# Kernel tuning notes

Hardware: AMD Instinct MI355X
Metric: run time of the kernel (lower is better)

Reference implementation:

```python
import jax, jax.numpy as jnp
import numpy as np


def setup_inputs() -> dict:
    key = jax.random.key(0)
    k1, k2 = jax.random.split(key)
    N, D, n_bags, per_bag = 8192, 512, 64, 128
    features = jax.random.normal(k1, (N, D), dtype=jnp.float32)
    # sorted bag indicator: 64 bags x 128 instances each
    batch = jnp.repeat(jnp.arange(n_bags, dtype=jnp.int32), per_bag)
    W = jax.random.normal(k2, (D, D), dtype=jnp.float32) * np.float32(1.0 / np.sqrt(D))
    b = jnp.zeros((D,), dtype=jnp.float32)
    return {"features": features, "W": W, "b": b, "batch": batch, "n_topk": 16, "n_bags": n_bags}


def reference(features, W, b, batch, n_topk, n_bags):
    N = features.shape[0]
    # F.normalize(dim=1): x / max(||x||, eps)
    norm = jnp.sqrt(jnp.sum(features * features, axis=1, keepdims=True))
    nf = features / jnp.maximum(norm, 1e-12)
    corr = nf @ nf.T  # [N, N] cosine-similarity map
    same_bag = batch[:, None] == batch[None, :]
    adj = jnp.where(same_bag, corr, 0.0)
    # scatter-zero the (N - n_topk) smallest per row == keep n_topk largest per row
    _, top_idx = jax.lax.top_k(adj, n_topk)  # [N, n_topk]
    keep = jnp.zeros((N, N), dtype=bool).at[jnp.arange(N)[:, None], top_idx].set(True)
    adj = jnp.where(keep, adj, 0.0)
    # dense_to_sparse()[0] keeps only indices -> unit edge weights for GCNConv.
    # GCNConv (gcn_norm, add_self_loops=True): A_hat = binarized adjacency with diag forced to 1.
    eye = jnp.eye(N, dtype=bool)
    A = jnp.where(eye, 1.0, (adj != 0).astype(features.dtype))  # [N, N]
    deg = jnp.sum(A, axis=0)  # degree scattered on target (col) index in PyG
    dis = jax.lax.rsqrt(deg)  # deg >= 1 thanks to self loops
    xw = features @ W  # [N, D]
    # out[col] = d[col]^-1/2 * sum_row A[row,col] * d[row]^-1/2 * xw[row]
    gcn_out = dis[:, None] * (A.T @ (dis[:, None] * xw)) + b
    # one-hot^T @ features == per-bag segment sum
    agg = jax.ops.segment_sum(gcn_out, batch, num_segments=n_bags)  # [n_bags, D]
    return agg, adj
```

## Files before the change

### kernel.cpp

```cpp
#include <hip/hip_runtime.h>
#include <hip/hip_bf16.h>

#define N 8192
#define D 512
#define NBAGS 64
#define PER_BAG 128
#define TOPK 16

typedef float vfloat4 __attribute__((ext_vector_type(4)));

#define WS_INVN   0
#define WS_KIDX   32768
#define WS_KCNT   557056
#define WS_DEG    589824

__global__ void norm_kernel(const float* __restrict__ feat,
                            float* __restrict__ invn,
                            int* __restrict__ deg) {
    int t = threadIdx.x;
    if (blockIdx.x < 32) deg[blockIdx.x * 256 + t] = 0;
    int lane = t & 63, w = t >> 6;
    int r = blockIdx.x * 4 + w;
    const float4* fr = (const float4*)(feat + (size_t)r * D);
    float4 a = fr[lane];
    float4 bq = fr[lane + 64];
    float ss = a.x * a.x + a.y * a.y + a.z * a.z + a.w * a.w
             + bq.x * bq.x + bq.y * bq.y + bq.z * bq.z + bq.w * bq.w;
    #pragma unroll
    for (int off = 32; off > 0; off >>= 1) ss += __shfl_down(ss, off);
    if (lane == 0) invn[r] = 1.0f / fmaxf(sqrtf(ss), 1e-12f);
}

__global__ __launch_bounds__(256, 1) void simtopk_kernel(
        const float* __restrict__ feat,
        const float* __restrict__ invn,
        float* __restrict__ adjOut,
        int* __restrict__ keptIdx,
        int* __restrict__ keptCnt,
        int* __restrict__ deg) {
    int rg = blockIdx.x;
    int bag = blockIdx.y;
    int t = threadIdx.x;
    __shared__ float colT[32][132];
    __shared__ float rowT[32][36];
    int bagBase = bag * PER_BAG;
    int rowBase = bagBase + rg * 32;
    int tx = t & 31;
    int ty = t >> 5;
    float4 acc[4];
    #pragma unroll
    for (int i = 0; i < 4; ++i) acc[i] = make_float4(0.f, 0.f, 0.f, 0.f);

    int kk = t & 31;
    int sub = t >> 5;
    int zrh = t >> 7;
    int zc  = t & 127;
    int jw  = bag >> 2;
    int winLo = bag * 32, winHi = winLo + 32;
    vfloat4 zf4 = {0.f, 0.f, 0.f, 0.f};

    for (int it = 0; it < 16; ++it) {
        int k0 = it * 32;
        __syncthreads();
        #pragma unroll
        for (int c0 = 0; c0 < 16; ++c0) {
            int c = sub * 16 + c0;
            colT[kk][c] = feat[(size_t)(bagBase + c) * D + k0 + kk];
        }
        #pragma unroll
        for (int r0 = 0; r0 < 4; ++r0) {
            int r = sub * 4 + r0;
            rowT[kk][r] = feat[(size_t)(rowBase + r) * D + k0 + kk];
        }
        __syncthreads();
        {
            int zr = 2 * it + zrh;
            vfloat4* rowp = (vfloat4*)(adjOut + (size_t)(rowBase + zr) * N);
            #pragma unroll
            for (int j = 0; j < 16; ++j) {
                int f = zc + 128 * j;
                if (j == jw) {
                    if (f < winLo || f >= winHi)
                        __builtin_nontemporal_store(zf4, &rowp[f]);
                } else {
                    __builtin_nontemporal_store(zf4, &rowp[f]);
                }
            }
        }
        #pragma unroll
        for (int k = 0; k < 32; ++k) {
            float4 cv = *(const float4*)&colT[k][4 * tx];
            float4 rv = *(const float4*)&rowT[k][4 * ty];
            acc[0].x += rv.x * cv.x; acc[0].y += rv.x * cv.y;
            acc[0].z += rv.x * cv.z; acc[0].w += rv.x * cv.w;
            acc[1].x += rv.y * cv.x; acc[1].y += rv.y * cv.y;
            acc[1].z += rv.y * cv.z; acc[1].w += rv.y * cv.w;
            acc[2].x += rv.z * cv.x; acc[2].y += rv.z * cv.y;
            acc[2].z += rv.z * cv.z; acc[2].w += rv.z * cv.w;
            acc[3].x += rv.w * cv.x; acc[3].y += rv.w * cv.y;
            acc[3].z += rv.w * cv.z; acc[3].w += rv.w * cv.w;
        }
    }
    float ic0 = invn[bagBase + 4 * tx];
    float ic1 = invn[bagBase + 4 * tx + 1];
    float ic2 = invn[bagBase + 4 * tx + 2];
    float ic3 = invn[bagBase + 4 * tx + 3];
    #pragma unroll
    for (int i = 0; i < 4; ++i) {
        float ir = invn[rowBase + 4 * ty + i];
        acc[i].x *= ir * ic0; acc[i].y *= ir * ic1;
        acc[i].z *= ir * ic2; acc[i].w *= ir * ic3;
    }
    #pragma unroll
    for (int i = 0; i < 4; ++i) {
        int r = rowBase + 4 * ty + i;
        float o0 = acc[i].x, o1 = acc[i].y, o2 = acc[i].z, o3 = acc[i].w;
        float w0 = o0, w1 = o1, w2 = o2, w3 = o3;
        int pm = 0, cnt = 0;
        #pragma unroll 1
        for (int itk = 0; itk < TOPK; ++itk) {
            float bv = w0; int bj = 0;
            if (w1 > bv) { bv = w1; bj = 1; }
            if (w2 > bv) { bv = w2; bj = 2; }
            if (w3 > bv) { bv = w3; bj = 3; }
            int bi = 4 * tx + bj;
            #pragma unroll
            for (int s = 1; s < 32; s <<= 1) {
                float ov = __shfl_xor(bv, s);
                int oi = __shfl_xor(bi, s);
                if (ov > bv || (ov == bv && oi < bi)) { bv = ov; bi = oi; }
            }
            if (bv <= 0.0f) break;
            if (tx == 0) keptIdx[(size_t)r * TOPK + cnt] = bi;
            cnt++;
            if ((bi >> 2) == tx) {
                pm |= 1 << (bi & 3);
                int q = bi & 3;
                if (q == 0) w0 = -1e30f;
                else if (q == 1) w1 = -1e30f;
                else if (q == 2) w2 = -1e30f;
                else w3 = -1e30f;
            }
        }
        if (tx == 0) keptCnt[r] = cnt;
        float4 ov4 = make_float4((pm & 1) ? o0 : 0.0f,
                                 (pm & 2) ? o1 : 0.0f,
                                 (pm & 4) ? o2 : 0.0f,
                                 (pm & 8) ? o3 : 0.0f);
        *(float4*)(adjOut + (size_t)r * N + bagBase + 4 * tx) = ov4;
        if (pm & 1) atomicAdd(&deg[bagBase + 4 * tx], 1);
        if (pm & 2) atomicAdd(&deg[bagBase + 4 * tx + 1], 1);
        if (pm & 4) atomicAdd(&deg[bagBase + 4 * tx + 2], 1);
        if (pm & 8) atomicAdd(&deg[bagBase + 4 * tx + 3], 1);
        int selfCol = rg * 32 + 4 * ty + i;
        if (tx == (selfCol >> 2) && !((pm >> (selfCol & 3)) & 1))
            atomicAdd(&deg[bagBase + selfCol], 1);
    }
}

__global__ void wfwagg_kernel(const float* __restrict__ feat,
                              const int* __restrict__ keptIdx,
                              const int* __restrict__ keptCnt,
                              const int* __restrict__ deg,
                              const float* __restrict__ Wm,
                              const float* __restrict__ b,
                              float* __restrict__ aggOut) {
    int bag = blockIdx.x;
    int t = threadIdx.x;
    __shared__ float wsh[PER_BAG];
    __shared__ float fws[D];
    int bagBase = bag * PER_BAG;
    if (t < PER_BAG) {
        int r = bagBase + t;
        int cnt = keptCnt[r];
        float sum = 0.0f;
        bool selfin = false;
        for (int k = 0; k < cnt; ++k) {
            int c = keptIdx[(size_t)r * TOPK + k];
            if (c == t) selfin = true;
            sum += rsqrtf((float)deg[bagBase + c]);
        }
        float disr = rsqrtf((float)deg[r]);
        if (!selfin) sum += disr;
        wsh[t] = disr * sum;
    }
    __syncthreads();
    float acc = 0.0f;
    #pragma unroll 8
    for (int r = 0; r < PER_BAG; ++r)
        acc += wsh[r] * feat[(size_t)(bagBase + r) * D + t];
    fws[t] = acc;
    __syncthreads();
    float acc2 = 0.0f;
    #pragma unroll 8
    for (int k = 0; k < D; ++k)
        acc2 += fws[k] * Wm[(size_t)k * D + t];
    aggOut[bag * D + t] = acc2 + 128.0f * b[t];
}

extern "C" void kernel_launch(void* const* d_in, const int* in_sizes, int n_in,
                              void* d_out, int out_size, void* d_ws, size_t ws_size,
                              hipStream_t stream) {
    const float* feat = (const float*)d_in[0];
    const float* Wm   = (const float*)d_in[1];
    const float* b    = (const float*)d_in[2];

    char* ws = (char*)d_ws;
    float* invn   = (float*)(ws + WS_INVN);
    int* keptIdx  = (int*)(ws + WS_KIDX);
    int* keptCnt  = (int*)(ws + WS_KCNT);
    int* deg      = (int*)(ws + WS_DEG);

    float* aggOut = (float*)d_out;
    float* adjOut = (float*)d_out + NBAGS * D;

    norm_kernel<<<N / 4, 256, 0, stream>>>(feat, invn, deg);
    simtopk_kernel<<<dim3(4, NBAGS), 256, 0, stream>>>(feat, invn, adjOut,
                                                       keptIdx, keptCnt, deg);
    wfwagg_kernel<<<NBAGS, 512, 0, stream>>>(feat, keptIdx, keptCnt, deg,
                                             Wm, b, aggOut);
}
```

Baseline: 367.5 us.

## Double-buffer similarity tile loads and split aggregation into parallel kernels

The similarity/top-k kernel now prefetches the next k-slice into registers with vectorized float4 loads while computing on a double-buffered shared tile, which removes one barrier per iteration and overlaps global loads with FMAs. The final weighted-feature and W projection stage is split into two kernels with more blocks (64x4 and 64x2) so more CUs participate instead of only 64 blocks. The split adds an extra kernel launch and a workspace round-trip for the intermediate vector.

New measurement: 371.4 us. No clear change (+1.1%).

```diff
diff --git a/kernel.cpp b/kernel.cpp
--- a/kernel.cpp
+++ b/kernel.cpp
@@ -13,6 +13,7 @@
 #define WS_KIDX   32768
 #define WS_KCNT   557056
 #define WS_DEG    589824
+#define WS_FW     622592
 
 __global__ void norm_kernel(const float* __restrict__ feat,
                             float* __restrict__ invn,
@@ -41,38 +42,60 @@
     int rg = blockIdx.x;
     int bag = blockIdx.y;
     int t = threadIdx.x;
-    __shared__ float colT[32][132];
-    __shared__ float rowT[32][36];
+    __shared__ float colT[2][32][132];
+    __shared__ float rowT[2][32][36];
     int bagBase = bag * PER_BAG;
     int rowBase = bagBase + rg * 32;
     int tx = t & 31;
     int ty = t >> 5;
+    const float4* feat4 = (const float4*)feat;
+
+    int cC[4], cKq[4];
+    #pragma unroll
+    for (int i = 0; i < 4; ++i) {
+        int fidx = i * 256 + t;
+        cC[i] = fidx >> 3;
+        cKq[i] = fidx & 7;
+    }
+    int rR = t >> 3, rKq = t & 7;
+
     float4 acc[4];
     #pragma unroll
     for (int i = 0; i < 4; ++i) acc[i] = make_float4(0.f, 0.f, 0.f, 0.f);
 
-    int kk = t & 31;
-    int sub = t >> 5;
     int zrh = t >> 7;
     int zc  = t & 127;
     int jw  = bag >> 2;
     int winLo = bag * 32, winHi = winLo + 32;
     vfloat4 zf4 = {0.f, 0.f, 0.f, 0.f};
 
+    float4 pc[4], pr;
+    #pragma unroll
+    for (int i = 0; i < 4; ++i)
+        pc[i] = feat4[(size_t)(bagBase + cC[i]) * 128 + cKq[i]];
+    pr = feat4[(size_t)(rowBase + rR) * 128 + rKq];
+
+    int buf = 0;
     for (int it = 0; it < 16; ++it) {
-        int k0 = it * 32;
+        #pragma unroll
+        for (int i = 0; i < 4; ++i) {
+            colT[buf][cKq[i] * 4 + 0][cC[i]] = pc[i].x;
+            colT[buf][cKq[i] * 4 + 1][cC[i]] = pc[i].y;
+            colT[buf][cKq[i] * 4 + 2][cC[i]] = pc[i].z;
+            colT[buf][cKq[i] * 4 + 3][cC[i]] = pc[i].w;
+        }
+        rowT[buf][rKq * 4 + 0][rR] = pr.x;
+        rowT[buf][rKq * 4 + 1][rR] = pr.y;
+        rowT[buf][rKq * 4 + 2][rR] = pr.z;
+        rowT[buf][rKq * 4 + 3][rR] = pr.w;
         __syncthreads();
-        #pragma unroll
-        for (int c0 = 0; c0 < 16; ++c0) {
-            int c = sub * 16 + c0;
-            colT[kk][c] = feat[(size_t)(bagBase + c) * D + k0 + kk];
-        }
-        #pragma unroll
-        for (int r0 = 0; r0 < 4; ++r0) {
-            int r = sub * 4 + r0;
-            rowT[kk][r] = feat[(size_t)(rowBase + r) * D + k0 + kk];
-        }
-        __syncthreads();
+        if (it < 15) {
+            int kq0 = (it + 1) * 8;
+            #pragma unroll
+            for (int i = 0; i < 4; ++i)
+                pc[i] = feat4[(size_t)(bagBase + cC[i]) * 128 + kq0 + cKq[i]];
+            pr = feat4[(size_t)(rowBase + rR) * 128 + kq0 + rKq];
+        }
         {
             int zr = 2 * it + zrh;
             vfloat4* rowp = (vfloat4*)(adjOut + (size_t)(rowBase + zr) * N);
@@ -87,19 +110,24 @@
                 }
             }
         }
-        #pragma unroll
-        for (int k = 0; k < 32; ++k) {
-            float4 cv = *(const float4*)&colT[k][4 * tx];
-            float4 rv = *(const float4*)&rowT[k][4 * ty];
-            acc[0].x += rv.x * cv.x; acc[0].y += rv.x * cv.y;
-            acc[0].z += rv.x * cv.z; acc[0].w += rv.x * cv.w;
-            acc[1].x += rv.y * cv.x; acc[1].y += rv.y * cv.y;
-            acc[1].z += rv.y * cv.z; acc[1].w += rv.y * cv.w;
-            acc[2].x += rv.z * cv.x; acc[2].y += rv.z * cv.y;
-            acc[2].z += rv.z * cv.z; acc[2].w += rv.z * cv.w;
-            acc[3].x += rv.w * cv.x; acc[3].y += rv.w * cv.y;
-            acc[3].z += rv.w * cv.z; acc[3].w += rv.w * cv.w;
-        }
+        {
+            const float (*cT)[132] = colT[buf];
+            const float (*rT)[36]  = rowT[buf];
+            #pragma unroll
+            for (int k = 0; k < 32; ++k) {
+                float4 cv = *(const float4*)&cT[k][4 * tx];
+                float4 rv = *(const float4*)&rT[k][4 * ty];
+                acc[0].x += rv.x * cv.x; acc[0].y += rv.x * cv.y;
+                acc[0].z += rv.x * cv.z; acc[0].w += rv.x * cv.w;
+                acc[1].x += rv.y * cv.x; acc[1].y += rv.y * cv.y;
+                acc[1].z += rv.y * cv.z; acc[1].w += rv.y * cv.w;
+                acc[2].x += rv.z * cv.x; acc[2].y += rv.z * cv.y;
+                acc[2].z += rv.z * cv.z; acc[2].w += rv.z * cv.w;
+                acc[3].x += rv.w * cv.x; acc[3].y += rv.w * cv.y;
+                acc[3].z += rv.w * cv.z; acc[3].w += rv.w * cv.w;
+            }
+        }
+        buf ^= 1;
     }
     float ic0 = invn[bagBase + 4 * tx];
     float ic1 = invn[bagBase + 4 * tx + 1];
@@ -158,19 +186,17 @@
     }
 }
 
-__global__ void wfwagg_kernel(const float* __restrict__ feat,
-                              const int* __restrict__ keptIdx,
-                              const int* __restrict__ keptCnt,
-                              const int* __restrict__ deg,
-                              const float* __restrict__ Wm,
-                              const float* __restrict__ b,
-                              float* __restrict__ aggOut) {
+__global__ void wfw_kernel(const float* __restrict__ feat,
+                           const int* __restrict__ keptIdx,
+                           const int* __restrict__ keptCnt,
+                           const int* __restrict__ deg,
+                           float* __restrict__ FW) {
     int bag = blockIdx.x;
+    int chunk = blockIdx.y;
     int t = threadIdx.x;
     __shared__ float wsh[PER_BAG];
-    __shared__ float fws[D];
     int bagBase = bag * PER_BAG;
-    if (t < PER_BAG) {
+    {
         int r = bagBase + t;
         int cnt = keptCnt[r];
         float sum = 0.0f;
@@ -185,17 +211,31 @@
         wsh[t] = disr * sum;
     }
     __syncthreads();
+    int d = chunk * 128 + t;
     float acc = 0.0f;
     #pragma unroll 8
     for (int r = 0; r < PER_BAG; ++r)
-        acc += wsh[r] * feat[(size_t)(bagBase + r) * D + t];
-    fws[t] = acc;
+        acc += wsh[r] * feat[(size_t)(bagBase + r) * D + d];
+    FW[bag * D + d] = acc;
+}
+
+__global__ void agg_kernel(const float* __restrict__ FW,
+                           const float* __restrict__ Wm,
+                           const float* __restrict__ b,
+                           float* __restrict__ aggOut) {
+    int bag = blockIdx.x;
+    int chunk = blockIdx.y;
+    int t = threadIdx.x;
+    __shared__ float fws[D];
+    fws[t] = FW[bag * D + t];
+    fws[256 + t] = FW[bag * D + 256 + t];
     __syncthreads();
-    float acc2 = 0.0f;
+    int d = chunk * 256 + t;
+    float acc = 0.0f;
     #pragma unroll 8
     for (int k = 0; k < D; ++k)
-        acc2 += fws[k] * Wm[(size_t)k * D + t];
-    aggOut[bag * D + t] = acc2 + 128.0f * b[t];
+        acc += fws[k] * Wm[(size_t)k * D + d];
+    aggOut[bag * D + d] = acc + 128.0f * b[d];
 }
 
 extern "C" void kernel_launch(void* const* d_in, const int* in_sizes, int n_in,
@@ -210,6 +250,7 @@
     int* keptIdx  = (int*)(ws + WS_KIDX);
     int* keptCnt  = (int*)(ws + WS_KCNT);
     int* deg      = (int*)(ws + WS_DEG);
+    float* FW     = (float*)(ws + WS_FW);
 
     float* aggOut = (float*)d_out;
     float* adjOut = (float*)d_out + NBAGS * D;
@@ -217,6 +258,7 @@
     norm_kernel<<<N / 4, 256, 0, stream>>>(feat, invn, deg);
     simtopk_kernel<<<dim3(4, NBAGS), 256, 0, stream>>>(feat, invn, adjOut,
                                                        keptIdx, keptCnt, deg);
-    wfwagg_kernel<<<NBAGS, 512, 0, stream>>>(feat, keptIdx, keptCnt, deg,
-                                             Wm, b, aggOut);
-}
+    wfw_kernel<<<dim3(NBAGS, 4), PER_BAG, 0, stream>>>(feat, keptIdx, keptCnt,
+                                                       deg, FW);
+    agg_kernel<<<dim3(NBAGS, 2), 256, 0, stream>>>(FW, Wm, b, aggOut);
+}
```

## Double simtopk grid with 16-row tiles and split wfwagg into two wider kernels

Applied to the files above, without the earlier changes.

The similarity/top-k kernel now handles 16 rows per block instead of 32, which doubles the grid to 512 blocks, and it raises the launch-bounds occupancy hint to 2 blocks per CU. The zero-fill of the 256 MB adjacency output is spread across more blocks in the same way. The final aggregation kernel, which used only 64 blocks, is split into a weighted-feature-sum kernel (64x4 blocks) and a W-projection kernel (64x2 blocks), with a workspace buffer between them. The aim is more parallelism and better store bandwidth. The cost is an extra launch and an intermediate round-trip, and each block now reloads the 128-column tile of its bag twice as often.

Result: faster. 353.3 us (-3.8%).

```diff
diff --git a/kernel.cpp b/kernel.cpp
--- a/kernel.cpp
+++ b/kernel.cpp
@@ -13,6 +13,7 @@
 #define WS_KIDX   32768
 #define WS_KCNT   557056
 #define WS_DEG    589824
+#define WS_FW     622592
 
 __global__ void norm_kernel(const float* __restrict__ feat,
                             float* __restrict__ invn,
@@ -31,7 +32,7 @@
     if (lane == 0) invn[r] = 1.0f / fmaxf(sqrtf(ss), 1e-12f);
 }
 
-__global__ __launch_bounds__(256, 1) void simtopk_kernel(
+__global__ __launch_bounds__(256, 2) void simtopk_kernel(
         const float* __restrict__ feat,
         const float* __restrict__ invn,
         float* __restrict__ adjOut,
@@ -42,20 +43,17 @@
     int bag = blockIdx.y;
     int t = threadIdx.x;
     __shared__ float colT[32][132];
-    __shared__ float rowT[32][36];
+    __shared__ float rowT[32][20];
     int bagBase = bag * PER_BAG;
-    int rowBase = bagBase + rg * 32;
+    int rowBase = bagBase + rg * 16;
     int tx = t & 31;
     int ty = t >> 5;
-    float4 acc[4];
-    #pragma unroll
-    for (int i = 0; i < 4; ++i) acc[i] = make_float4(0.f, 0.f, 0.f, 0.f);
+    float4 acc0 = make_float4(0.f, 0.f, 0.f, 0.f);
+    float4 acc1 = make_float4(0.f, 0.f, 0.f, 0.f);
 
     int kk = t & 31;
     int sub = t >> 5;
-    int zrh = t >> 7;
-    int zc  = t & 127;
-    int jw  = bag >> 2;
+    int jw = bag >> 3;
     int winLo = bag * 32, winHi = winLo + 32;
     vfloat4 zf4 = {0.f, 0.f, 0.f, 0.f};
 
@@ -68,17 +66,16 @@
             colT[kk][c] = feat[(size_t)(bagBase + c) * D + k0 + kk];
         }
         #pragma unroll
-        for (int r0 = 0; r0 < 4; ++r0) {
-            int r = sub * 4 + r0;
+        for (int r0 = 0; r0 < 2; ++r0) {
+            int r = sub * 2 + r0;
             rowT[kk][r] = feat[(size_t)(rowBase + r) * D + k0 + kk];
         }
         __syncthreads();
         {
-            int zr = 2 * it + zrh;
-            vfloat4* rowp = (vfloat4*)(adjOut + (size_t)(rowBase + zr) * N);
+            vfloat4* rowp = (vfloat4*)(adjOut + (size_t)(rowBase + it) * N);
             #pragma unroll
-            for (int j = 0; j < 16; ++j) {
-                int f = zc + 128 * j;
+            for (int j = 0; j < 8; ++j) {
+                int f = t + 256 * j;
                 if (j == jw) {
                     if (f < winLo || f >= winHi)
                         __builtin_nontemporal_store(zf4, &rowp[f]);
@@ -90,31 +87,30 @@
         #pragma unroll
         for (int k = 0; k < 32; ++k) {
             float4 cv = *(const float4*)&colT[k][4 * tx];
-            float4 rv = *(const float4*)&rowT[k][4 * ty];
-            acc[0].x += rv.x * cv.x; acc[0].y += rv.x * cv.y;
-            acc[0].z += rv.x * cv.z; acc[0].w += rv.x * cv.w;
-            acc[1].x += rv.y * cv.x; acc[1].y += rv.y * cv.y;
-            acc[1].z += rv.y * cv.z; acc[1].w += rv.y * cv.w;
-            acc[2].x += rv.z * cv.x; acc[2].y += rv.z * cv.y;
-            acc[2].z += rv.z * cv.z; acc[2].w += rv.z * cv.w;
-            acc[3].x += rv.w * cv.x; acc[3].y += rv.w * cv.y;
-            acc[3].z += rv.w * cv.z; acc[3].w += rv.w * cv.w;
+            float rv0 = rowT[k][2 * ty];
+            float rv1 = rowT[k][2 * ty + 1];
+            acc0.x += rv0 * cv.x; acc0.y += rv0 * cv.y;
+            acc0.z += rv0 * cv.z; acc0.w += rv0 * cv.w;
+            acc1.x += rv1 * cv.x; acc1.y += rv1 * cv.y;
+            acc1.z += rv1 * cv.z; acc1.w += rv1 * cv.w;
         }
     }
     float ic0 = invn[bagBase + 4 * tx];
     float ic1 = invn[bagBase + 4 * tx + 1];
     float ic2 = invn[bagBase + 4 * tx + 2];
     float ic3 = invn[bagBase + 4 * tx + 3];
+    float ir0 = invn[rowBase + 2 * ty];
+    float ir1 = invn[rowBase + 2 * ty + 1];
+    acc0.x *= ir0 * ic0; acc0.y *= ir0 * ic1;
+    acc0.z *= ir0 * ic2; acc0.w *= ir0 * ic3;
+    acc1.x *= ir1 * ic0; acc1.y *= ir1 * ic1;
+    acc1.z *= ir1 * ic2; acc1.w *= ir1 * ic3;
+
     #pragma unroll
-    for (int i = 0; i < 4; ++i) {
-        float ir = invn[rowBase + 4 * ty + i];
-        acc[i].x *= ir * ic0; acc[i].y *= ir * ic1;
-        acc[i].z *= ir * ic2; acc[i].w *= ir * ic3;
-    }
-    #pragma unroll
-    for (int i = 0; i < 4; ++i) {
-        int r = rowBase + 4 * ty + i;
-        float o0 = acc[i].x, o1 = acc[i].y, o2 = acc[i].z, o3 = acc[i].w;
+    for (int i = 0; i < 2; ++i) {
+        int r = rowBase + 2 * ty + i;
+        float4 a4 = i ? acc1 : acc0;
+        float o0 = a4.x, o1 = a4.y, o2 = a4.z, o3 = a4.w;
         float w0 = o0, w1 = o1, w2 = o2, w3 = o3;
         int pm = 0, cnt = 0;
         #pragma unroll 1
@@ -152,25 +148,23 @@
         if (pm & 2) atomicAdd(&deg[bagBase + 4 * tx + 1], 1);
         if (pm & 4) atomicAdd(&deg[bagBase + 4 * tx + 2], 1);
         if (pm & 8) atomicAdd(&deg[bagBase + 4 * tx + 3], 1);
-        int selfCol = rg * 32 + 4 * ty + i;
+        int selfCol = rg * 16 + 2 * ty + i;
         if (tx == (selfCol >> 2) && !((pm >> (selfCol & 3)) & 1))
             atomicAdd(&deg[bagBase + selfCol], 1);
     }
 }
 
-__global__ void wfwagg_kernel(const float* __restrict__ feat,
-                              const int* __restrict__ keptIdx,
-                              const int* __restrict__ keptCnt,
-                              const int* __restrict__ deg,
-                              const float* __restrict__ Wm,
-                              const float* __restrict__ b,
-                              float* __restrict__ aggOut) {
+__global__ void wfw_kernel(const float* __restrict__ feat,
+                           const int* __restrict__ keptIdx,
+                           const int* __restrict__ keptCnt,
+                           const int* __restrict__ deg,
+                           float* __restrict__ FW) {
     int bag = blockIdx.x;
+    int chunk = blockIdx.y;
     int t = threadIdx.x;
     __shared__ float wsh[PER_BAG];
-    __shared__ float fws[D];
     int bagBase = bag * PER_BAG;
-    if (t < PER_BAG) {
+    {
         int r = bagBase + t;
         int cnt = keptCnt[r];
         float sum = 0.0f;
@@ -185,17 +179,31 @@
         wsh[t] = disr * sum;
     }
     __syncthreads();
+    int d = chunk * 128 + t;
     float acc = 0.0f;
     #pragma unroll 8
     for (int r = 0; r < PER_BAG; ++r)
-        acc += wsh[r] * feat[(size_t)(bagBase + r) * D + t];
-    fws[t] = acc;
+        acc += wsh[r] * feat[(size_t)(bagBase + r) * D + d];
+    FW[bag * D + d] = acc;
+}
+
+__global__ void agg_kernel(const float* __restrict__ FW,
+                           const float* __restrict__ Wm,
+                           const float* __restrict__ b,
+                           float* __restrict__ aggOut) {
+    int bag = blockIdx.x;
+    int chunk = blockIdx.y;
+    int t = threadIdx.x;
+    __shared__ float fws[D];
+    fws[t] = FW[bag * D + t];
+    fws[256 + t] = FW[bag * D + 256 + t];
     __syncthreads();
-    float acc2 = 0.0f;
+    int d = chunk * 256 + t;
+    float acc = 0.0f;
     #pragma unroll 8
     for (int k = 0; k < D; ++k)
-        acc2 += fws[k] * Wm[(size_t)k * D + t];
-    aggOut[bag * D + t] = acc2 + 128.0f * b[t];
+        acc += fws[k] * Wm[(size_t)k * D + d];
+    aggOut[bag * D + d] = acc + 128.0f * b[d];
 }
 
 extern "C" void kernel_launch(void* const* d_in, const int* in_sizes, int n_in,
@@ -210,13 +218,15 @@
     int* keptIdx  = (int*)(ws + WS_KIDX);
     int* keptCnt  = (int*)(ws + WS_KCNT);
     int* deg      = (int*)(ws + WS_DEG);
+    float* FW     = (float*)(ws + WS_FW);
 
     float* aggOut = (float*)d_out;
     float* adjOut = (float*)d_out + NBAGS * D;
 
     norm_kernel<<<N / 4, 256, 0, stream>>>(feat, invn, deg);
-    simtopk_kernel<<<dim3(4, NBAGS), 256, 0, stream>>>(feat, invn, adjOut,
+    simtopk_kernel<<<dim3(8, NBAGS), 256, 0, stream>>>(feat, invn, adjOut,
                                                        keptIdx, keptCnt, deg);
-    wfwagg_kernel<<<NBAGS, 512, 0, stream>>>(feat, keptIdx, keptCnt, deg,
-                                             Wm, b, aggOut);
-}
+    wfw_kernel<<<dim3(NBAGS, 4), PER_BAG, 0, stream>>>(feat, keptIdx, keptCnt,
+                                                       deg, FW);
+    agg_kernel<<<dim3(NBAGS, 2), 256, 0, stream>>>(FW, Wm, b, aggOut);
+}
```
